# Kernel tuning notes

Hardware: AMD Instinct MI355X
Metric: run time of the kernel (lower is better)

Reference implementation:

```python
import jax, jax.numpy as jnp
import numpy as np

N_NODES = 100000
N_EDGES = 1600000
IN_CH = 128
HID = 128
EMBED = 256
NUM_GRAPHS = 128


def setup_inputs() -> dict:
    key = jax.random.key(0)
    ks = jax.random.split(key, 12)
    x = jax.random.normal(ks[0], (N_NODES, IN_CH), dtype=jnp.float32)
    edge_index = jax.random.randint(ks[1], (2, N_EDGES), 0, N_NODES, dtype=jnp.int64)
    batch = jnp.sort(jax.random.randint(ks[2], (N_NODES,), 0, NUM_GRAPHS, dtype=jnp.int64))
    s = 0.05
    # conv1 MLP: Linear(in_ch,128) -> ReLU -> Linear(128,128)
    W11 = jax.random.normal(ks[3], (IN_CH, HID), dtype=jnp.float32) * s
    b11 = jnp.zeros((HID,), dtype=jnp.float32)
    W12 = jax.random.normal(ks[4], (HID, HID), dtype=jnp.float32) * s
    b12 = jnp.zeros((HID,), dtype=jnp.float32)
    # conv2 MLP: Linear(128,128) -> ReLU -> Linear(128,embed)
    W21 = jax.random.normal(ks[5], (HID, HID), dtype=jnp.float32) * s
    b21 = jnp.zeros((HID,), dtype=jnp.float32)
    W22 = jax.random.normal(ks[6], (HID, EMBED), dtype=jnp.float32) * s
    b22 = jnp.zeros((EMBED,), dtype=jnp.float32)
    gamma = jnp.ones((EMBED,), dtype=jnp.float32)
    beta = jnp.zeros((EMBED,), dtype=jnp.float32)
    return {"x": x, "edge_index": edge_index, "batch": batch,
            "W11": W11, "b11": b11, "W12": W12, "b12": b12,
            "W21": W21, "b21": b21, "W22": W22, "b22": b22,
            "gamma": gamma, "beta": beta}


def _gin_conv(x, src, dst, W_a, b_a, W_b, b_b):
    # GINConv with eps=0: MLP(x + sum_{j in N(i)} x_j)
    msgs = x[src]                                   # [E, d] gather
    agg = jax.ops.segment_sum(msgs, dst, num_segments=N_NODES)  # scatter-add
    h = x + agg
    h = jax.nn.relu(h @ W_a + b_a)
    return h @ W_b + b_b


def reference(x, edge_index, batch, W11, b11, W12, b12, W21, b21, W22, b22, gamma, beta):
    src, dst = edge_index[0], edge_index[1]
    h = jax.nn.relu(_gin_conv(x, src, dst, W11, b11, W12, b12))   # [N, 128]
    h = jax.nn.relu(_gin_conv(h, src, dst, W21, b21, W22, b22))   # [N, 256]
    # global_mean_pool over graphs
    sums = jax.ops.segment_sum(h, batch, num_segments=NUM_GRAPHS)           # [G, 256]
    counts = jax.ops.segment_sum(jnp.ones((N_NODES,), h.dtype), batch, num_segments=NUM_GRAPHS)
    pooled = sums / jnp.maximum(counts, 1.0)[:, None]
    # LayerNorm over last dim (eps=1e-5 as in torch)
    mu = jnp.mean(pooled, axis=-1, keepdims=True)
    var = jnp.var(pooled, axis=-1, keepdims=True)
    out = (pooled - mu) * jax.lax.rsqrt(var + 1e-5) * gamma + beta
    # Dropout in eval mode: identity
    return out
```

## Files before the change

kernel.cpp:

```cpp
#include <hip/hip_runtime.h>

#define GRAPHS 128
#define CHUNKC 4000

typedef _Float16 f16x8 __attribute__((ext_vector_type(8)));
typedef _Float16 f16x4 __attribute__((ext_vector_type(4)));
typedef _Float16 f16x2 __attribute__((ext_vector_type(2)));
typedef float f32x4 __attribute__((ext_vector_type(4)));

__device__ __forceinline__ void fmix_lo(float& a, int w) {
  asm("v_fma_mix_f32 %0, %1, 1.0, %0 op_sel:[0,0,0] op_sel_hi:[1,0,0]" : "+v"(a) : "v"(w));
}
__device__ __forceinline__ void fmix_hi(float& a, int w) {
  asm("v_fma_mix_f32 %0, %1, 1.0, %0 op_sel:[1,0,0] op_sel_hi:[1,0,0]" : "+v"(a) : "v"(w));
}

__device__ __forceinline__ void gload_lds16(const void* g, void* l) {
  __builtin_amdgcn_global_load_lds((const __attribute__((address_space(1))) void*)g,
                                   (__attribute__((address_space(3))) void*)l, 16, 0, 0);
}

__global__ void k_prep(const int* __restrict__ dst, int* __restrict__ histG,
                       int e, int NB, int NW,
                       const float* __restrict__ x, _Float16* __restrict__ P0,
                       _Float16* __restrict__ P1, int n,
                       const float* __restrict__ W11, const float* __restrict__ W12,
                       const float* __restrict__ W21, const float* __restrict__ W22,
                       f16x8* __restrict__ f11, f16x8* __restrict__ f12,
                       f16x8* __restrict__ f21, f16x8* __restrict__ f22,
                       float* __restrict__ pool, int cvtb, int wpb, int poolb) {
  __shared__ int h[256];
  int b = blockIdx.x, t = threadIdx.x;
  if (b < NW) {
    h[t] = 0; __syncthreads();
    int lo = b * CHUNKC, hi = min(lo + CHUNKC, e);
    for (int i = lo + t; i < hi; i += 256) atomicAdd(&h[dst[i] >> 9], 1);
    __syncthreads();
    if (t < NB) histG[t * NW + b] = h[t];
    return;
  }
  b -= NW;
  if (b < cvtb) {
    int i = b * 256 + t;
    if (i < n * 32) {
      float4 v = ((const float4*)x)[i];
      f16x4 hh = { (_Float16)v.x, (_Float16)v.y, (_Float16)v.z, (_Float16)v.w };
      ((f16x4*)P0)[i] = hh;
    }
    return;
  }
  b -= cvtb;
  if (b < wpb) {
    int id = b * 256 + t;
    const float* W; f16x8* F; int C, cid, fshift;
    if (id < 2048)       { W = W11; F = f11; C = 128; cid = id;        fshift = 3; }
    else if (id < 4096)  { W = W12; F = f12; C = 128; cid = id - 2048; fshift = 3; }
    else if (id < 6144)  { W = W21; F = f21; C = 128; cid = id - 4096; fshift = 3; }
    else if (id < 10240) { W = W22; F = f22; C = 256; cid = id - 6144; fshift = 4; }
    else return;
    int lane = cid & 63;
    int rest = cid >> 6;
    int fc = rest & ((1 << fshift) - 1);
    int kk = rest >> fshift;
    int cout = fc * 16 + (lane & 15);
    int kb = kk * 32 + (lane >> 4) * 8;
    f16x8 v;
#pragma unroll
    for (int q = 0; q < 8; ++q) v[q] = (_Float16)W[(size_t)(kb + q) * C + cout];
    F[cid] = v;
    return;
  }
  b -= wpb;
  if (b < poolb) {
    int i = b * 256 + t;
    if (i < GRAPHS * 256) pool[i] = 0.f;
    return;
  }
  if (t < 128) P0[(size_t)n * 128 + t] = (_Float16)0.f;
  else P1[(size_t)n * 128 + (t - 128)] = (_Float16)0.f;
}

__global__ void k_scanA(const int* __restrict__ in, int* __restrict__ out,
                        int* __restrict__ bsum, int N) {
  __shared__ int s[256];
  int t = threadIdx.x, b = blockIdx.x;
  int base = b * 1024 + t * 4;
  int v[4]; int tot = 0;
#pragma unroll
  for (int j = 0; j < 4; ++j) { int i = base + j; v[j] = (i < N) ? in[i] : 0; tot += v[j]; }
  s[t] = tot; __syncthreads();
  for (int o = 1; o < 256; o <<= 1) {
    int x = (t >= o) ? s[t - o] : 0;
    __syncthreads(); s[t] += x; __syncthreads();
  }
  int run = s[t] - tot;
#pragma unroll
  for (int j = 0; j < 4; ++j) { int i = base + j; if (i < N) out[i] = run; run += v[j]; }
  if (t == 255) bsum[b] = s[255];
}

__global__ void k_scanB(int* bsum, int nb, const int* __restrict__ batch,
                        int* __restrict__ starts, int n) {
  __shared__ int s[256];
  int t = threadIdx.x;
  int v = (t < nb) ? bsum[t] : 0;
  s[t] = v; __syncthreads();
  for (int o = 1; o < 256; o <<= 1) {
    int x = (t >= o) ? s[t - o] : 0;
    __syncthreads(); s[t] += x; __syncthreads();
  }
  if (t < nb) bsum[t] = s[t] - v;
  if (t <= GRAPHS) {
    int lo = 0, hi = n;
    while (lo < hi) { int mid = (lo + hi) >> 1; if (batch[mid] < t) lo = mid + 1; else hi = mid; }
    starts[t] = lo;
  }
}

__global__ void k_part(const int* __restrict__ src, const int* __restrict__ dst,
                       const int* __restrict__ histG, const int* __restrict__ off,
                       const int* __restrict__ bsum,
                       int* __restrict__ part, int e, int NB, int NW) {
  __shared__ int hist[256], lbA[256], lbB[256], stmp[256];
  __shared__ int els[CHUNKC];
  int t = threadIdx.x, w = blockIdx.x;
  int hv = (t < NB) ? histG[t * NW + w] : 0;
  hist[t] = hv; stmp[t] = hv; __syncthreads();
  for (int o = 1; o < 256; o <<= 1) {
    int x = (t >= o) ? stmp[t - o] : 0;
    __syncthreads(); stmp[t] += x; __syncthreads();
  }
  lbA[t] = stmp[t] - hv; lbB[t] = stmp[t] - hv;
  __syncthreads();
  int lo = w * CHUNKC, hi = min(lo + CHUNKC, e);
  for (int i = lo + t; i < hi; i += 256) {
    int d = dst[i];
    int p = atomicAdd(&lbB[d >> 9], 1);
    els[p] = src[i] | ((d & 511) << 17);
  }
  __syncthreads();
  int ln = t & 63, wv = t >> 6;
  for (int b = wv; b < NB; b += 4) {
    int c = hist[b], lb = lbA[b];
    int idx = b * NW + w;
    long g = off[idx] + bsum[idx >> 10];
    for (int j = ln; j < c; j += 64) part[g + j] = els[lb + j];
  }
}

__global__ void k_csrb(const int* __restrict__ part, const int* __restrict__ off,
                       const int* __restrict__ bsum,
                       int* __restrict__ ptr, int* __restrict__ csr,
                       int e, int NB, int NW, int n) {
  __shared__ int nh[512], ncur[512], stmp[256];
  int t = threadIdx.x, b = blockIdx.x;
  int i0 = b * NW;
  int s0 = off[i0] + bsum[i0 >> 10];
  int e0 = e;
  if (b + 1 < NB) { int i1 = (b + 1) * NW; e0 = off[i1] + bsum[i1 >> 10]; }
  nh[t] = 0; nh[t + 256] = 0; __syncthreads();
  for (int i = s0 + t; i < e0; i += 256) atomicAdd(&nh[((unsigned)part[i]) >> 17], 1);
  __syncthreads();
  int v0 = nh[2 * t], v1 = nh[2 * t + 1];
  int ps = v0 + v1;
  stmp[t] = ps; __syncthreads();
  for (int o = 1; o < 256; o <<= 1) {
    int x = (t >= o) ? stmp[t - o] : 0;
    __syncthreads(); stmp[t] += x; __syncthreads();
  }
  int base = stmp[t] - ps;
  __syncthreads();
  nh[2 * t] = base;   nh[2 * t + 1] = base + v0;
  ncur[2 * t] = base; ncur[2 * t + 1] = base + v0;
  __syncthreads();
#pragma unroll
  for (int q = 0; q < 2; ++q) {
    int vv = t + q * 256;
    int node = (b << 9) + vv;
    if (node <= n) ptr[node] = s0 + nh[vv];
  }
  for (int i = s0 + t; i < e0; i += 256) {
    int u = part[i];
    int p = atomicAdd(&ncur[((unsigned)u) >> 17], 1);
    csr[s0 + p] = u & 0x1FFFF;
  }
}

__global__ void k_agg_h(const _Float16* __restrict__ in, _Float16* __restrict__ out,
                        const int* __restrict__ ptr, const int* __restrict__ csr, int n) {
  int gid = blockIdx.x * 256 + threadIdx.x;
  int node = gid >> 6, lane = gid & 63;
  if (node >= n) return;
  const f16x8* inp = (const f16x8*)in;
  int cb = lane & 15, rg = lane >> 4;
  f16x8 self = inp[(size_t)node * 16 + cb];
  float acc[8];
#pragma unroll
  for (int c = 0; c < 8; ++c) acc[c] = (rg == 0) ? (float)self[c] : 0.f;
  int s = ptr[node], deg = ptr[node + 1] - s;
  union W { f16x8 v; int i[4]; };
  for (int seg = 0; seg < deg; seg += 64) {
    int my = (seg + lane < deg) ? csr[s + seg + lane] : n;
    int segn = min(deg - seg, 64);
    for (int b2 = 0; b2 < segn; b2 += 32) {
      int jj[8]; W w[8];
#pragma unroll
      for (int u = 0; u < 8; ++u) jj[u] = __shfl(my, b2 + u * 4 + rg);
#pragma unroll
      for (int u = 0; u < 8; ++u) w[u].v = inp[(size_t)jj[u] * 16 + cb];
#pragma unroll
      for (int u = 0; u < 8; ++u)
#pragma unroll
        for (int p = 0; p < 4; ++p) {
          fmix_lo(acc[2 * p], w[u].i[p]);
          fmix_hi(acc[2 * p + 1], w[u].i[p]);
        }
    }
  }
#pragma unroll
  for (int c = 0; c < 8; ++c) {
    acc[c] += __shfl_xor(acc[c], 16);
    acc[c] += __shfl_xor(acc[c], 32);
  }
  if (rg == 0) {
    f16x8 r;
#pragma unroll
    for (int c = 0; c < 8; ++c) r[c] = (_Float16)acc[c];
    ((f16x8*)out)[(size_t)node * 16 + cb] = r;
  }
}

__device__ __forceinline__ f16x8 xpose(f32x4 aE, f32x4 aO, int rg) {
  union U2 { _Float16 h[2]; int i; };
  union U8 { int i[4]; f16x8 v; };
  U2 e01, e23, o01, o23;
  e01.h[0] = (_Float16)aE[0]; e01.h[1] = (_Float16)aE[1];
  e23.h[0] = (_Float16)aE[2]; e23.h[1] = (_Float16)aE[3];
  o01.h[0] = (_Float16)aO[0]; o01.h[1] = (_Float16)aO[1];
  o23.h[0] = (_Float16)aO[2]; o23.h[1] = (_Float16)aO[3];
  int e01x1 = __shfl_xor(e01.i, 16), e01x2 = __shfl_xor(e01.i, 32), e01x3 = __shfl_xor(e01.i, 48);
  int e23x1 = __shfl_xor(e23.i, 16), e23x2 = __shfl_xor(e23.i, 32), e23x3 = __shfl_xor(e23.i, 48);
  int o01x1 = __shfl_xor(o01.i, 16), o01x2 = __shfl_xor(o01.i, 32), o01x3 = __shfl_xor(o01.i, 48);
  int o23x1 = __shfl_xor(o23.i, 16), o23x2 = __shfl_xor(o23.i, 32), o23x3 = __shfl_xor(o23.i, 48);
  U8 r;
  r.i[0] = rg == 0 ? e01.i : rg == 1 ? e01x3 : rg == 2 ? o01x2 : o01x1;
  r.i[1] = rg == 0 ? e23.i : rg == 1 ? e23x3 : rg == 2 ? o23x2 : o23x1;
  r.i[2] = rg == 0 ? e01x1 : rg == 1 ? e01x2 : rg == 2 ? o01x3 : o01.i;
  r.i[3] = rg == 0 ? e23x1 : rg == 1 ? e23x2 : rg == 2 ? o23x3 : o23.i;
  return r.v;
}

__launch_bounds__(256, 2)
__global__ void k_mlp128(const _Float16* __restrict__ in, const f16x8* __restrict__ wfA,
                         const float* __restrict__ bA, const f16x8* __restrict__ wfB,
                         const float* __restrict__ bB, _Float16* __restrict__ out, int n) {
  __shared__ f16x8 wa[2048];
  __shared__ f16x8 wb[2048];
  int t = threadIdx.x;
  int r0 = blockIdx.x * 128;
  int lane = t & 63, w = t >> 6;
  int l16 = lane & 15, rg = lane >> 4;
  int rw = w * 32;
  const f16x8* inp = (const f16x8*)in;
  int ra0 = r0 + rw + l16;      if (ra0 > n) ra0 = n;
  int ra1 = r0 + rw + 16 + l16; if (ra1 > n) ra1 = n;
  f16x8 xf[2][4];
#pragma unroll
  for (int kk = 0; kk < 4; ++kk) {
    xf[0][kk] = inp[(size_t)ra0 * 16 + kk * 4 + rg];
    xf[1][kk] = inp[(size_t)ra1 * 16 + kk * 4 + rg];
  }
#pragma unroll
  for (int i = 0; i < 8; ++i) {
    int base = i * 256 + w * 64;
    gload_lds16(&wfA[base + lane], &wa[base]);
    gload_lds16(&wfB[base + lane], &wb[base]);
  }
  __syncthreads();
  f32x4 acc[2][8];
#pragma unroll
  for (int rs = 0; rs < 2; ++rs)
#pragma unroll
    for (int fc = 0; fc < 8; ++fc) acc[rs][fc] = (f32x4){0.f, 0.f, 0.f, 0.f};
#pragma unroll
  for (int kk = 0; kk < 4; ++kk)
#pragma unroll
    for (int fc = 0; fc < 8; ++fc) {
      f16x8 a = wa[(kk * 8 + fc) * 64 + lane];
      acc[0][fc] = __builtin_amdgcn_mfma_f32_16x16x32_f16(a, xf[0][kk], acc[0][fc], 0, 0, 0);
      acc[1][fc] = __builtin_amdgcn_mfma_f32_16x16x32_f16(a, xf[1][kk], acc[1][fc], 0, 0, 0);
    }
  f16x8 hf[2][4];
#pragma unroll
  for (int fc = 0; fc < 8; ++fc) {
    float4 bv = *(const float4*)(bA + fc * 16 + rg * 4);
#pragma unroll
    for (int rs = 0; rs < 2; ++rs) {
      acc[rs][fc][0] = fmaxf(acc[rs][fc][0] + bv.x, 0.f);
      acc[rs][fc][1] = fmaxf(acc[rs][fc][1] + bv.y, 0.f);
      acc[rs][fc][2] = fmaxf(acc[rs][fc][2] + bv.z, 0.f);
      acc[rs][fc][3] = fmaxf(acc[rs][fc][3] + bv.w, 0.f);
    }
  }
#pragma unroll
  for (int rs = 0; rs < 2; ++rs)
#pragma unroll
    for (int kk = 0; kk < 4; ++kk)
      hf[rs][kk] = xpose(acc[rs][2 * kk], acc[rs][2 * kk + 1], rg);
#pragma unroll
  for (int rs = 0; rs < 2; ++rs)
#pragma unroll
    for (int fc = 0; fc < 8; ++fc) acc[rs][fc] = (f32x4){0.f, 0.f, 0.f, 0.f};
#pragma unroll
  for (int kk = 0; kk < 4; ++kk)
#pragma unroll
    for (int fc = 0; fc < 8; ++fc) {
      f16x8 b = wb[(kk * 8 + fc) * 64 + lane];
      acc[0][fc] = __builtin_amdgcn_mfma_f32_16x16x32_f16(b, hf[0][kk], acc[0][fc], 0, 0, 0);
      acc[1][fc] = __builtin_amdgcn_mfma_f32_16x16x32_f16(b, hf[1][kk], acc[1][fc], 0, 0, 0);
    }
#pragma unroll
  for (int fc = 0; fc < 8; ++fc) {
    float4 bv = *(const float4*)(bB + fc * 16 + rg * 4);
#pragma unroll
    for (int rs = 0; rs < 2; ++rs) {
      acc[rs][fc][0] = fmaxf(acc[rs][fc][0] + bv.x, 0.f);
      acc[rs][fc][1] = fmaxf(acc[rs][fc][1] + bv.y, 0.f);
      acc[rs][fc][2] = fmaxf(acc[rs][fc][2] + bv.z, 0.f);
      acc[rs][fc][3] = fmaxf(acc[rs][fc][3] + bv.w, 0.f);
    }
  }
  f16x8* outp = (f16x8*)out;
#pragma unroll
  for (int rs = 0; rs < 2; ++rs) {
    int row = r0 + rw + rs * 16 + l16;
#pragma unroll
    for (int kk = 0; kk < 4; ++kk) {
      f16x8 o = xpose(acc[rs][2 * kk], acc[rs][2 * kk + 1], rg);
      if (row < n) outp[(size_t)row * 16 + kk * 4 + rg] = o;
    }
  }
}

__launch_bounds__(256, 2)
__global__ void k_mlp_pool(const _Float16* __restrict__ in, const f16x8* __restrict__ wfA,
                           const float* __restrict__ bA, const f16x8* __restrict__ wfB,
                           const float* __restrict__ bB, const int* __restrict__ batch,
                           float* __restrict__ pool, int n) {
  __shared__ f16x8 wa[2048];
  __shared__ f16x8 wb[2048];
  __shared__ float pool_l[8 * 128];
  int t = threadIdx.x;
  int h = blockIdx.x & 1;
  int r0 = (blockIdx.x >> 1) * 128;
  int lane = t & 63, w = t >> 6;
  int l16 = lane & 15, rg = lane >> 4;
  int rw = w * 32;
  const f16x8* inp = (const f16x8*)in;
#pragma unroll
  for (int j = 0; j < 4; ++j) pool_l[j * 256 + t] = 0.f;
  int ra0 = r0 + rw + l16;      if (ra0 > n) ra0 = n;
  int ra1 = r0 + rw + 16 + l16; if (ra1 > n) ra1 = n;
  f16x8 xf[2][4];
#pragma unroll
  for (int kk = 0; kk < 4; ++kk) {
    xf[0][kk] = inp[(size_t)ra0 * 16 + kk * 4 + rg];
    xf[1][kk] = inp[(size_t)ra1 * 16 + kk * 4 + rg];
  }
  int g0 = batch[r0];
  int rloc = rw + rg * 4;
  int g4[2][4];
#pragma unroll
  for (int fr = 0; fr < 2; ++fr)
#pragma unroll
    for (int j = 0; j < 4; ++j) {
      int row = r0 + rloc + fr * 16 + j;
      g4[fr][j] = (row < n) ? batch[row] : -1;
    }
#pragma unroll
  for (int i = 0; i < 8; ++i) {
    int base = i * 256 + w * 64;
    gload_lds16(&wfA[base + lane], &wa[base]);
    int fcl = (i * 4 + w) & 7, kk = (i * 4 + w) >> 3;
    gload_lds16(&wfB[(kk * 16 + h * 8 + fcl) * 64 + lane], &wb[base]);
  }
  __syncthreads();
  f32x4 acc[2][8];
#pragma unroll
  for (int rs = 0; rs < 2; ++rs)
#pragma unroll
    for (int fc = 0; fc < 8; ++fc) acc[rs][fc] = (f32x4){0.f, 0.f, 0.f, 0.f};
#pragma unroll
  for (int kk = 0; kk < 4; ++kk)
#pragma unroll
    for (int fc = 0; fc < 8; ++fc) {
      f16x8 a = wa[(kk * 8 + fc) * 64 + lane];
      acc[0][fc] = __builtin_amdgcn_mfma_f32_16x16x32_f16(a, xf[0][kk], acc[0][fc], 0, 0, 0);
      acc[1][fc] = __builtin_amdgcn_mfma_f32_16x16x32_f16(a, xf[1][kk], acc[1][fc], 0, 0, 0);
    }
  f16x8 hf[2][4];
#pragma unroll
  for (int fc = 0; fc < 8; ++fc) {
    float4 bv = *(const float4*)(bA + fc * 16 + rg * 4);
#pragma unroll
    for (int rs = 0; rs < 2; ++rs) {
      acc[rs][fc][0] = fmaxf(acc[rs][fc][0] + bv.x, 0.f);
      acc[rs][fc][1] = fmaxf(acc[rs][fc][1] + bv.y, 0.f);
      acc[rs][fc][2] = fmaxf(acc[rs][fc][2] + bv.z, 0.f);
      acc[rs][fc][3] = fmaxf(acc[rs][fc][3] + bv.w, 0.f);
    }
  }
#pragma unroll
  for (int rs = 0; rs < 2; ++rs)
#pragma unroll
    for (int kk = 0; kk < 4; ++kk)
      hf[rs][kk] = xpose(acc[rs][2 * kk], acc[rs][2 * kk + 1], rg);
#pragma unroll
  for (int rs = 0; rs < 2; ++rs)
#pragma unroll
    for (int fc = 0; fc < 8; ++fc) acc[rs][fc] = (f32x4){0.f, 0.f, 0.f, 0.f};
#pragma unroll
  for (int kk = 0; kk < 4; ++kk)
#pragma unroll
    for (int fc = 0; fc < 8; ++fc) {
      f16x8 b = wb[(kk * 8 + fc) * 64 + lane];
      acc[0][fc] = __builtin_amdgcn_mfma_f32_16x16x32_f16(hf[0][kk], b, acc[0][fc], 0, 0, 0);
      acc[1][fc] = __builtin_amdgcn_mfma_f32_16x16x32_f16(hf[1][kk], b, acc[1][fc], 0, 0, 0);
    }
#pragma unroll
  for (int fc = 0; fc < 8; ++fc) {
    int col128 = fc * 16 + l16;
    float bv = bB[h * 128 + col128];
#pragma unroll
    for (int fr = 0; fr < 2; ++fr) {
      f32x4 a = acc[fr][fc];
      float run = fmaxf(a[0] + bv, 0.f);
#pragma unroll
      for (int j = 1; j < 4; ++j) {
        float v = fmaxf(a[j] + bv, 0.f);
        if (g4[fr][j] == g4[fr][j - 1]) run += v;
        else {
          int g = g4[fr][j - 1];
          if (g >= 0) {
            int d = g - g0;
            if (d >= 0 && d < 8) atomicAdd(&pool_l[d * 128 + col128], run);
            else atomicAdd(&pool[g * 256 + h * 128 + col128], run);
          }
          run = v;
        }
      }
      int g = g4[fr][3];
      if (g >= 0) {
        int d = g - g0;
        if (d >= 0 && d < 8) atomicAdd(&pool_l[d * 128 + col128], run);
        else atomicAdd(&pool[g * 256 + h * 128 + col128], run);
      }
    }
  }
  __syncthreads();
#pragma unroll
  for (int j = 0; j < 4; ++j) {
    int idx = j * 256 + t;
    int g = g0 + (idx >> 7), col128 = idx & 127;
    float v = pool_l[idx];
    if (g < GRAPHS && v != 0.f) atomicAdd(&pool[g * 256 + h * 128 + col128], v);
  }
}

__global__ void k_final(const float* __restrict__ pool, const int* __restrict__ starts,
                        const float* __restrict__ gamma, const float* __restrict__ beta,
                        float* __restrict__ out) {
  __shared__ float2 red[256];
  int g = blockIdx.x, ch = threadIdx.x;
  int cnt = starts[g + 1] - starts[g];
  float p = pool[g * 256 + ch] / fmaxf((float)cnt, 1.f);
  red[ch] = make_float2(p, p * p);
  __syncthreads();
  for (int off = 128; off > 0; off >>= 1) {
    if (ch < off) { red[ch].x += red[ch + off].x; red[ch].y += red[ch + off].y; }
    __syncthreads();
  }
  float mu = red[0].x * (1.f / 256.f);
  float var = red[0].y * (1.f / 256.f) - mu * mu;
  out[g * 256 + ch] = (p - mu) * rsqrtf(var + 1e-5f) * gamma[ch] + beta[ch];
}

extern "C" void kernel_launch(void* const* d_in, const int* in_sizes, int n_in,
                              void* d_out, int out_size, void* d_ws, size_t ws_size,
                              hipStream_t stream) {
  const float* x     = (const float*)d_in[0];
  const int*   ei    = (const int*)d_in[1];
  const int*   batch = (const int*)d_in[2];
  const float* W11 = (const float*)d_in[3];  const float* b11 = (const float*)d_in[4];
  const float* W12 = (const float*)d_in[5];  const float* b12 = (const float*)d_in[6];
  const float* W21 = (const float*)d_in[7];  const float* b21 = (const float*)d_in[8];
  const float* W22 = (const float*)d_in[9];  const float* b22 = (const float*)d_in[10];
  const float* gamma = (const float*)d_in[11];
  const float* beta  = (const float*)d_in[12];
  float* out = (float*)d_out;

  int n = in_sizes[0] / 128;
  int e = in_sizes[1] / 2;
  const int* src = ei;
  const int* dstv = ei + e;

  int NB = (n + 511) >> 9;
  int NW = (e + CHUNKC - 1) / CHUNKC;
  int NS = NB * NW;
  int mb = (n + 127) / 128;

  char* ws = (char*)d_ws;
  auto alloc = [&](size_t bytes) { char* p = ws; ws += (bytes + 15) & ~(size_t)15; return p; };
  _Float16* P0 = (_Float16*)alloc((size_t)(n + 1) * 128 * 2);
  _Float16* P1 = (_Float16*)alloc((size_t)(n + 1) * 128 * 2);
  float* pool  = (float*)alloc((size_t)GRAPHS * 256 * 4);
  int* ptr     = (int*)alloc((size_t)(n + 1) * 4);
  int* csr     = (int*)alloc((size_t)e * 4);
  int* part    = (int*)alloc((size_t)e * 4);
  int* histG   = (int*)alloc((size_t)NS * 4);
  int* off     = (int*)alloc((size_t)NS * 4);
  int* bsum    = (int*)alloc(256 * 4);
  int* starts  = (int*)alloc((GRAPHS + 1) * 4);
  f16x8* f11 = (f16x8*)alloc(2048 * 16);
  f16x8* f12 = (f16x8*)alloc(2048 * 16);
  f16x8* f21 = (f16x8*)alloc(2048 * 16);
  f16x8* f22 = (f16x8*)alloc(4096 * 16);

  int cvtb = (n * 32 + 255) / 256;
  int wpb = 40;
  int poolb = (GRAPHS * 256 + 255) / 256;
  int prepb = NW + cvtb + wpb + poolb + 1;

  int nbk = (NS + 1023) / 1024;
  k_prep <<<prepb, 256, 0, stream>>>(dstv, histG, e, NB, NW, x, P0, P1, n,
                                     W11, W12, W21, W22, f11, f12, f21, f22,
                                     pool, cvtb, wpb, poolb);
  k_scanA<<<nbk, 256, 0, stream>>>(histG, off, bsum, NS);
  k_scanB<<<1, 256, 0, stream>>>(bsum, nbk, batch, starts, n);
  k_part <<<NW, 256, 0, stream>>>(src, dstv, histG, off, bsum, part, e, NB, NW);
  k_csrb <<<NB, 256, 0, stream>>>(part, off, bsum, ptr, csr, e, NB, NW, n);

  int ab = (n * 64 + 255) / 256;

  k_agg_h<<<ab, 256, 0, stream>>>(P0, P1, ptr, csr, n);
  k_mlp128<<<mb, 256, 0, stream>>>(P1, f11, b11, f12, b12, P0, n);
  k_agg_h<<<ab, 256, 0, stream>>>(P0, P1, ptr, csr, n);
  k_mlp_pool<<<mb * 2, 256, 0, stream>>>(P1, f21, b21, f22, b22, batch, pool, n);
  k_final<<<GRAPHS, 256, 0, stream>>>(pool, starts, gamma, beta, out);
}
```

Before: 282.1 us.

## Fuse neighbor aggregation into MLP kernels and drop separate gather passes

Removes the standalone aggregation kernels and performs the CSR neighbor sum directly inside the MLP kernels, producing MFMA input fragments in registers. The pool kernel now handles both output halves in one block, reloading the second weight half into LDS instead of launching twice as many blocks. This avoids writing and rereading the aggregated feature buffer and two launches, at the cost of far fewer threads doing the gather, each walking neighbor lists serially with limited memory parallelism.

```diff
diff --git a/kernel.cpp b/kernel.cpp
--- a/kernel.cpp
+++ b/kernel.cpp
@@ -5,7 +5,6 @@
 
 typedef _Float16 f16x8 __attribute__((ext_vector_type(8)));
 typedef _Float16 f16x4 __attribute__((ext_vector_type(4)));
-typedef _Float16 f16x2 __attribute__((ext_vector_type(2)));
 typedef float f32x4 __attribute__((ext_vector_type(4)));
 
 __device__ __forceinline__ void fmix_lo(float& a, int w) {
@@ -186,50 +185,6 @@
   }
 }
 
-__global__ void k_agg_h(const _Float16* __restrict__ in, _Float16* __restrict__ out,
-                        const int* __restrict__ ptr, const int* __restrict__ csr, int n) {
-  int gid = blockIdx.x * 256 + threadIdx.x;
-  int node = gid >> 6, lane = gid & 63;
-  if (node >= n) return;
-  const f16x8* inp = (const f16x8*)in;
-  int cb = lane & 15, rg = lane >> 4;
-  f16x8 self = inp[(size_t)node * 16 + cb];
-  float acc[8];
-#pragma unroll
-  for (int c = 0; c < 8; ++c) acc[c] = (rg == 0) ? (float)self[c] : 0.f;
-  int s = ptr[node], deg = ptr[node + 1] - s;
-  union W { f16x8 v; int i[4]; };
-  for (int seg = 0; seg < deg; seg += 64) {
-    int my = (seg + lane < deg) ? csr[s + seg + lane] : n;
-    int segn = min(deg - seg, 64);
-    for (int b2 = 0; b2 < segn; b2 += 32) {
-      int jj[8]; W w[8];
-#pragma unroll
-      for (int u = 0; u < 8; ++u) jj[u] = __shfl(my, b2 + u * 4 + rg);
-#pragma unroll
-      for (int u = 0; u < 8; ++u) w[u].v = inp[(size_t)jj[u] * 16 + cb];
-#pragma unroll
-      for (int u = 0; u < 8; ++u)
-#pragma unroll
-        for (int p = 0; p < 4; ++p) {
-          fmix_lo(acc[2 * p], w[u].i[p]);
-          fmix_hi(acc[2 * p + 1], w[u].i[p]);
-        }
-    }
-  }
-#pragma unroll
-  for (int c = 0; c < 8; ++c) {
-    acc[c] += __shfl_xor(acc[c], 16);
-    acc[c] += __shfl_xor(acc[c], 32);
-  }
-  if (rg == 0) {
-    f16x8 r;
-#pragma unroll
-    for (int c = 0; c < 8; ++c) r[c] = (_Float16)acc[c];
-    ((f16x8*)out)[(size_t)node * 16 + cb] = r;
-  }
-}
-
 __device__ __forceinline__ f16x8 xpose(f32x4 aE, f32x4 aO, int rg) {
   union U2 { _Float16 h[2]; int i; };
   union U8 { int i[4]; f16x8 v; };
@@ -250,10 +205,71 @@
   return r.v;
 }
 
+__device__ __forceinline__ void agg_frag(const f16x8* __restrict__ inp,
+                                         const int* __restrict__ ptr,
+                                         const int* __restrict__ csr,
+                                         int node, int rg, int n, f16x8* xf) {
+  if (node >= n) {
+#pragma unroll
+    for (int kk = 0; kk < 4; ++kk) xf[kk] = (f16x8){0,0,0,0,0,0,0,0};
+    return;
+  }
+  float acc[4][8];
+#pragma unroll
+  for (int kk = 0; kk < 4; ++kk) {
+    f16x8 v = inp[(size_t)node * 16 + kk * 4 + rg];
+#pragma unroll
+    for (int q = 0; q < 8; ++q) acc[kk][q] = (float)v[q];
+  }
+  int s = ptr[node], d = ptr[node + 1] - s;
+  union W { f16x8 v; int i[4]; };
+  int i = 0;
+  for (; i + 2 <= d; i += 2) {
+    int j0 = csr[s + i], j1 = csr[s + i + 1];
+    W a0[4], a1[4];
+#pragma unroll
+    for (int kk = 0; kk < 4; ++kk) {
+      a0[kk].v = inp[(size_t)j0 * 16 + kk * 4 + rg];
+      a1[kk].v = inp[(size_t)j1 * 16 + kk * 4 + rg];
+    }
+#pragma unroll
+    for (int kk = 0; kk < 4; ++kk)
+#pragma unroll
+      for (int p = 0; p < 4; ++p) {
+        fmix_lo(acc[kk][2 * p], a0[kk].i[p]);
+        fmix_hi(acc[kk][2 * p + 1], a0[kk].i[p]);
+        fmix_lo(acc[kk][2 * p], a1[kk].i[p]);
+        fmix_hi(acc[kk][2 * p + 1], a1[kk].i[p]);
+      }
+  }
+  if (i < d) {
+    int j0 = csr[s + i];
+    W a0[4];
+#pragma unroll
+    for (int kk = 0; kk < 4; ++kk) a0[kk].v = inp[(size_t)j0 * 16 + kk * 4 + rg];
+#pragma unroll
+    for (int kk = 0; kk < 4; ++kk)
+#pragma unroll
+      for (int p = 0; p < 4; ++p) {
+        fmix_lo(acc[kk][2 * p], a0[kk].i[p]);
+        fmix_hi(acc[kk][2 * p + 1], a0[kk].i[p]);
+      }
+  }
+#pragma unroll
+  for (int kk = 0; kk < 4; ++kk) {
+    f16x8 r;
+#pragma unroll
+    for (int q = 0; q < 8; ++q) r[q] = (_Float16)acc[kk][q];
+    xf[kk] = r;
+  }
+}
+
 __launch_bounds__(256, 2)
-__global__ void k_mlp128(const _Float16* __restrict__ in, const f16x8* __restrict__ wfA,
-                         const float* __restrict__ bA, const f16x8* __restrict__ wfB,
-                         const float* __restrict__ bB, _Float16* __restrict__ out, int n) {
+__global__ void k_agg_mlp(const _Float16* __restrict__ in, const int* __restrict__ ptr,
+                          const int* __restrict__ csr,
+                          const f16x8* __restrict__ wfA, const float* __restrict__ bA,
+                          const f16x8* __restrict__ wfB, const float* __restrict__ bB,
+                          _Float16* __restrict__ out, int n) {
   __shared__ f16x8 wa[2048];
   __shared__ f16x8 wb[2048];
   int t = threadIdx.x;
@@ -262,20 +278,15 @@
   int l16 = lane & 15, rg = lane >> 4;
   int rw = w * 32;
   const f16x8* inp = (const f16x8*)in;
-  int ra0 = r0 + rw + l16;      if (ra0 > n) ra0 = n;
-  int ra1 = r0 + rw + 16 + l16; if (ra1 > n) ra1 = n;
-  f16x8 xf[2][4];
-#pragma unroll
-  for (int kk = 0; kk < 4; ++kk) {
-    xf[0][kk] = inp[(size_t)ra0 * 16 + kk * 4 + rg];
-    xf[1][kk] = inp[(size_t)ra1 * 16 + kk * 4 + rg];
-  }
 #pragma unroll
   for (int i = 0; i < 8; ++i) {
     int base = i * 256 + w * 64;
     gload_lds16(&wfA[base + lane], &wa[base]);
     gload_lds16(&wfB[base + lane], &wb[base]);
   }
+  f16x8 xf[2][4];
+  agg_frag(inp, ptr, csr, r0 + rw + l16, rg, n, xf[0]);
+  agg_frag(inp, ptr, csr, r0 + rw + 16 + l16, rg, n, xf[1]);
   __syncthreads();
   f32x4 acc[2][8];
 #pragma unroll
@@ -343,29 +354,29 @@
 }
 
 __launch_bounds__(256, 2)
-__global__ void k_mlp_pool(const _Float16* __restrict__ in, const f16x8* __restrict__ wfA,
-                           const float* __restrict__ bA, const f16x8* __restrict__ wfB,
-                           const float* __restrict__ bB, const int* __restrict__ batch,
-                           float* __restrict__ pool, int n) {
+__global__ void k_agg_mlp_pool(const _Float16* __restrict__ in, const int* __restrict__ ptr,
+                               const int* __restrict__ csr,
+                               const f16x8* __restrict__ wfA, const float* __restrict__ bA,
+                               const f16x8* __restrict__ wfB, const float* __restrict__ bB,
+                               const int* __restrict__ batch, float* __restrict__ pool, int n) {
   __shared__ f16x8 wa[2048];
   __shared__ f16x8 wb[2048];
-  __shared__ float pool_l[8 * 128];
+  __shared__ float pool_l[8 * 256];
   int t = threadIdx.x;
-  int h = blockIdx.x & 1;
-  int r0 = (blockIdx.x >> 1) * 128;
+  int r0 = blockIdx.x * 128;
   int lane = t & 63, w = t >> 6;
   int l16 = lane & 15, rg = lane >> 4;
   int rw = w * 32;
   const f16x8* inp = (const f16x8*)in;
 #pragma unroll
-  for (int j = 0; j < 4; ++j) pool_l[j * 256 + t] = 0.f;
-  int ra0 = r0 + rw + l16;      if (ra0 > n) ra0 = n;
-  int ra1 = r0 + rw + 16 + l16; if (ra1 > n) ra1 = n;
-  f16x8 xf[2][4];
-#pragma unroll
-  for (int kk = 0; kk < 4; ++kk) {
-    xf[0][kk] = inp[(size_t)ra0 * 16 + kk * 4 + rg];
-    xf[1][kk] = inp[(size_t)ra1 * 16 + kk * 4 + rg];
+  for (int j = 0; j < 8; ++j) pool_l[j * 256 + t] = 0.f;
+#pragma unroll
+  for (int i = 0; i < 8; ++i) {
+    int base = i * 256 + w * 64;
+    gload_lds16(&wfA[base + lane], &wa[base]);
+    int grp = i * 4 + w;
+    int fcl = grp & 7, kk = grp >> 3;
+    gload_lds16(&wfB[(kk * 16 + fcl) * 64 + lane], &wb[base]);
   }
   int g0 = batch[r0];
   int rloc = rw + rg * 4;
@@ -377,13 +388,9 @@
       int row = r0 + rloc + fr * 16 + j;
       g4[fr][j] = (row < n) ? batch[row] : -1;
     }
-#pragma unroll
-  for (int i = 0; i < 8; ++i) {
-    int base = i * 256 + w * 64;
-    gload_lds16(&wfA[base + lane], &wa[base]);
-    int fcl = (i * 4 + w) & 7, kk = (i * 4 + w) >> 3;
-    gload_lds16(&wfB[(kk * 16 + h * 8 + fcl) * 64 + lane], &wb[base]);
-  }
+  f16x8 xf[2][4];
+  agg_frag(inp, ptr, csr, r0 + rw + l16, rg, n, xf[0]);
+  agg_frag(inp, ptr, csr, r0 + rw + 16 + l16, rg, n, xf[1]);
   __syncthreads();
   f32x4 acc[2][8];
 #pragma unroll
@@ -415,55 +422,68 @@
 #pragma unroll
     for (int kk = 0; kk < 4; ++kk)
       hf[rs][kk] = xpose(acc[rs][2 * kk], acc[rs][2 * kk + 1], rg);
-#pragma unroll
-  for (int rs = 0; rs < 2; ++rs)
-#pragma unroll
-    for (int fc = 0; fc < 8; ++fc) acc[rs][fc] = (f32x4){0.f, 0.f, 0.f, 0.f};
-#pragma unroll
-  for (int kk = 0; kk < 4; ++kk)
+  for (int h = 0; h < 2; ++h) {
+    if (h) {
+      __syncthreads();
+#pragma unroll
+      for (int i = 0; i < 8; ++i) {
+        int base = i * 256 + w * 64;
+        int grp = i * 4 + w;
+        int fcl = grp & 7, kk = grp >> 3;
+        gload_lds16(&wfB[(kk * 16 + 8 + fcl) * 64 + lane], &wb[base]);
+      }
+      __syncthreads();
+    }
+#pragma unroll
+    for (int rs = 0; rs < 2; ++rs)
+#pragma unroll
+      for (int fc = 0; fc < 8; ++fc) acc[rs][fc] = (f32x4){0.f, 0.f, 0.f, 0.f};
+#pragma unroll
+    for (int kk = 0; kk < 4; ++kk)
+#pragma unroll
+      for (int fc = 0; fc < 8; ++fc) {
+        f16x8 b = wb[(kk * 8 + fc) * 64 + lane];
+        acc[0][fc] = __builtin_amdgcn_mfma_f32_16x16x32_f16(hf[0][kk], b, acc[0][fc], 0, 0, 0);
+        acc[1][fc] = __builtin_amdgcn_mfma_f32_16x16x32_f16(hf[1][kk], b, acc[1][fc], 0, 0, 0);
+      }
 #pragma unroll
     for (int fc = 0; fc < 8; ++fc) {
-      f16x8 b = wb[(kk * 8 + fc) * 64 + lane];
-      acc[0][fc] = __builtin_amdgcn_mfma_f32_16x16x32_f16(hf[0][kk], b, acc[0][fc], 0, 0, 0);
-      acc[1][fc] = __builtin_amdgcn_mfma_f32_16x16x32_f16(hf[1][kk], b, acc[1][fc], 0, 0, 0);
-    }
-#pragma unroll
-  for (int fc = 0; fc < 8; ++fc) {
-    int col128 = fc * 16 + l16;
-    float bv = bB[h * 128 + col128];
-#pragma unroll
-    for (int fr = 0; fr < 2; ++fr) {
-      f32x4 a = acc[fr][fc];
-      float run = fmaxf(a[0] + bv, 0.f);
-#pragma unroll
-      for (int j = 1; j < 4; ++j) {
-        float v = fmaxf(a[j] + bv, 0.f);
-        if (g4[fr][j] == g4[fr][j - 1]) run += v;
-        else {
-          int g = g4[fr][j - 1];
-          if (g >= 0) {
-            int d = g - g0;
-            if (d >= 0 && d < 8) atomicAdd(&pool_l[d * 128 + col128], run);
-            else atomicAdd(&pool[g * 256 + h * 128 + col128], run);
+      int col = h * 128 + fc * 16 + l16;
+      float bv = bB[col];
+#pragma unroll
+      for (int fr = 0; fr < 2; ++fr) {
+        f32x4 a = acc[fr][fc];
+        float run = fmaxf(a[0] + bv, 0.f);
+#pragma unroll
+        for (int j = 1; j < 4; ++j) {
+          float v = fmaxf(a[j] + bv, 0.f);
+          if (g4[fr][j] == g4[fr][j - 1]) run += v;
+          else {
+            int g = g4[fr][j - 1];
+            if (g >= 0) {
+              int d = g - g0;
+              if (d >= 0 && d < 8) atomicAdd(&pool_l[d * 256 + col], run);
+              else atomicAdd(&pool[g * 256 + col], run);
+            }
+            run = v;
           }
-          run = v;
+        }
+        int g = g4[fr][3];
+        if (g >= 0) {
+          int d = g - g0;
+          if (d >= 0 && d < 8) atomicAdd(&pool_l[d * 256 + col], run);
+          else atomicAdd(&pool[g * 256 + col], run);
         }
       }
-      int g = g4[fr][3];
-      if (g >= 0) {
-        int d = g - g0;
-        if (d >= 0 && d < 8) atomicAdd(&pool_l[d * 128 + col128], run);
-        else atomicAdd(&pool[g * 256 + h * 128 + col128], run);
-      }
-    }
-  }
-  __syncthreads();
-#pragma unroll
-  for (int j = 0; j < 4; ++j) {
+    }
+  }
+  __syncthreads();
+#pragma unroll
+  for (int j = 0; j < 8; ++j) {
     int idx = j * 256 + t;
-    int g = g0 + (idx >> 7), col128 = idx & 127;
+    int g = g0 + (idx >> 8), col = idx & 255;
     float v = pool_l[idx];
-    if (g < GRAPHS && v != 0.f) atomicAdd(&pool[g * 256 + h * 128 + col128], v);
+    if (g < GRAPHS && v != 0.f) atomicAdd(&pool[g * 256 + col], v);
   }
 }
 
@@ -540,11 +560,7 @@
   k_part <<<NW, 256, 0, stream>>>(src, dstv, histG, off, bsum, part, e, NB, NW);
   k_csrb <<<NB, 256, 0, stream>>>(part, off, bsum, ptr, csr, e, NB, NW, n);
 
-  int ab = (n * 64 + 255) / 256;
-
-  k_agg_h<<<ab, 256, 0, stream>>>(P0, P1, ptr, csr, n);
-  k_mlp128<<<mb, 256, 0, stream>>>(P1, f11, b11, f12, b12, P0, n);
-  k_agg_h<<<ab, 256, 0, stream>>>(P0, P1, ptr, csr, n);
-  k_mlp_pool<<<mb * 2, 256, 0, stream>>>(P1, f21, b21, f22, b22, batch, pool, n);
+  k_agg_mlp<<<mb, 256, 0, stream>>>(P0, ptr, csr, f11, b11, f12, b12, P1, n);
+  k_agg_mlp_pool<<<mb, 256, 0, stream>>>(P1, ptr, csr, f21, b21, f22, b22, batch, pool, n);
   k_final<<<GRAPHS, 256, 0, stream>>>(pool, starts, gamma, beta, out);
 }
```

Measured after the change: 310.6 us. 10.1% more time.

## Process four row tiles per block in MLP kernels to amortize weight loads

Applied to the files above, without the earlier changes.

Each MLP block now loads its weight fragments into LDS once and loops over four consecutive 128-row tiles instead of one, cutting the grid by a factor of four. The direct global-to-LDS loads are replaced by plain register-staged copies. The pool kernel now uses a per-block graph base computed from its first tile for the local pool buffer, and a graph that falls outside that 8-graph window goes to global atomics. The aim is to cut redundant weight traffic and block setup, at the cost of fewer blocks in flight (about 196 for the first MLP) and less latency hiding within each block.

```diff
diff --git a/kernel.cpp b/kernel.cpp
--- a/kernel.cpp
+++ b/kernel.cpp
@@ -5,7 +5,6 @@
 
 typedef _Float16 f16x8 __attribute__((ext_vector_type(8)));
 typedef _Float16 f16x4 __attribute__((ext_vector_type(4)));
-typedef _Float16 f16x2 __attribute__((ext_vector_type(2)));
 typedef float f32x4 __attribute__((ext_vector_type(4)));
 
 __device__ __forceinline__ void fmix_lo(float& a, int w) {
@@ -13,11 +12,6 @@
 }
 __device__ __forceinline__ void fmix_hi(float& a, int w) {
   asm("v_fma_mix_f32 %0, %1, 1.0, %0 op_sel:[1,0,0] op_sel_hi:[1,0,0]" : "+v"(a) : "v"(w));
-}
-
-__device__ __forceinline__ void gload_lds16(const void* g, void* l) {
-  __builtin_amdgcn_global_load_lds((const __attribute__((address_space(1))) void*)g,
-                                   (__attribute__((address_space(3))) void*)l, 16, 0, 0);
 }
 
 __global__ void k_prep(const int* __restrict__ dst, int* __restrict__ histG,
@@ -253,91 +247,97 @@
 __launch_bounds__(256, 2)
 __global__ void k_mlp128(const _Float16* __restrict__ in, const f16x8* __restrict__ wfA,
                          const float* __restrict__ bA, const f16x8* __restrict__ wfB,
-                         const float* __restrict__ bB, _Float16* __restrict__ out, int n) {
+                         const float* __restrict__ bB, _Float16* __restrict__ out,
+                         int n, int mb) {
   __shared__ f16x8 wa[2048];
   __shared__ f16x8 wb[2048];
   int t = threadIdx.x;
-  int r0 = blockIdx.x * 128;
   int lane = t & 63, w = t >> 6;
   int l16 = lane & 15, rg = lane >> 4;
   int rw = w * 32;
   const f16x8* inp = (const f16x8*)in;
-  int ra0 = r0 + rw + l16;      if (ra0 > n) ra0 = n;
-  int ra1 = r0 + rw + 16 + l16; if (ra1 > n) ra1 = n;
-  f16x8 xf[2][4];
-#pragma unroll
-  for (int kk = 0; kk < 4; ++kk) {
-    xf[0][kk] = inp[(size_t)ra0 * 16 + kk * 4 + rg];
-    xf[1][kk] = inp[(size_t)ra1 * 16 + kk * 4 + rg];
-  }
+  f16x8* outp = (f16x8*)out;
 #pragma unroll
   for (int i = 0; i < 8; ++i) {
-    int base = i * 256 + w * 64;
-    gload_lds16(&wfA[base + lane], &wa[base]);
-    gload_lds16(&wfB[base + lane], &wb[base]);
-  }
-  __syncthreads();
-  f32x4 acc[2][8];
-#pragma unroll
-  for (int rs = 0; rs < 2; ++rs)
-#pragma unroll
-    for (int fc = 0; fc < 8; ++fc) acc[rs][fc] = (f32x4){0.f, 0.f, 0.f, 0.f};
-#pragma unroll
-  for (int kk = 0; kk < 4; ++kk)
+    wa[t + i * 256] = wfA[t + i * 256];
+    wb[t + i * 256] = wfB[t + i * 256];
+  }
+  __syncthreads();
+  int t0 = blockIdx.x * 4;
+#pragma unroll 1
+  for (int it = 0; it < 4; ++it) {
+    int tile = t0 + it;
+    if (tile >= mb) break;
+    int r0 = tile * 128;
+    int ra0 = r0 + rw + l16;      if (ra0 > n) ra0 = n;
+    int ra1 = r0 + rw + 16 + l16; if (ra1 > n) ra1 = n;
+    f16x8 xf[2][4];
+#pragma unroll
+    for (int kk = 0; kk < 4; ++kk) {
+      xf[0][kk] = inp[(size_t)ra0 * 16 + kk * 4 + rg];
+      xf[1][kk] = inp[(size_t)ra1 * 16 + kk * 4 + rg];
+    }
+    f32x4 acc[2][8];
+#pragma unroll
+    for (int rs = 0; rs < 2; ++rs)
+#pragma unroll
+      for (int fc = 0; fc < 8; ++fc) acc[rs][fc] = (f32x4){0.f, 0.f, 0.f, 0.f};
+#pragma unroll
+    for (int kk = 0; kk < 4; ++kk)
+#pragma unroll
+      for (int fc = 0; fc < 8; ++fc) {
+        f16x8 a = wa[(kk * 8 + fc) * 64 + lane];
+        acc[0][fc] = __builtin_amdgcn_mfma_f32_16x16x32_f16(a, xf[0][kk], acc[0][fc], 0, 0, 0);
+        acc[1][fc] = __builtin_amdgcn_mfma_f32_16x16x32_f16(a, xf[1][kk], acc[1][fc], 0, 0, 0);
+      }
+    f16x8 hf[2][4];
 #pragma unroll
     for (int fc = 0; fc < 8; ++fc) {
-      f16x8 a = wa[(kk * 8 + fc) * 64 + lane];
-      acc[0][fc] = __builtin_amdgcn_mfma_f32_16x16x32_f16(a, xf[0][kk], acc[0][fc], 0, 0, 0);
-      acc[1][fc] = __builtin_amdgcn_mfma_f32_16x16x32_f16(a, xf[1][kk], acc[1][fc], 0, 0, 0);
-    }
-  f16x8 hf[2][4];
-#pragma unroll
-  for (int fc = 0; fc < 8; ++fc) {
-    float4 bv = *(const float4*)(bA + fc * 16 + rg * 4);
+      float4 bv = *(const float4*)(bA + fc * 16 + rg * 4);
+#pragma unroll
+      for (int rs = 0; rs < 2; ++rs) {
+        acc[rs][fc][0] = fmaxf(acc[rs][fc][0] + bv.x, 0.f);
+        acc[rs][fc][1] = fmaxf(acc[rs][fc][1] + bv.y, 0.f);
+        acc[rs][fc][2] = fmaxf(acc[rs][fc][2] + bv.z, 0.f);
+        acc[rs][fc][3] = fmaxf(acc[rs][fc][3] + bv.w, 0.f);
+      }
+    }
+#pragma unroll
+    for (int rs = 0; rs < 2; ++rs)
+#pragma unroll
+      for (int kk = 0; kk < 4; ++kk)
+        hf[rs][kk] = xpose(acc[rs][2 * kk], acc[rs][2 * kk + 1], rg);
+#pragma unroll
+    for (int rs = 0; rs < 2; ++rs)
+#pragma unroll
+      for (int fc = 0; fc < 8; ++fc) acc[rs][fc] = (f32x4){0.f, 0.f, 0.f, 0.f};
+#pragma unroll
+    for (int kk = 0; kk < 4; ++kk)
+#pragma unroll
+      for (int fc = 0; fc < 8; ++fc) {
+        f16x8 b = wb[(kk * 8 + fc) * 64 + lane];
+        acc[0][fc] = __builtin_amdgcn_mfma_f32_16x16x32_f16(b, hf[0][kk], acc[0][fc], 0, 0, 0);
+        acc[1][fc] = __builtin_amdgcn_mfma_f32_16x16x32_f16(b, hf[1][kk], acc[1][fc], 0, 0, 0);
+      }
+#pragma unroll
+    for (int fc = 0; fc < 8; ++fc) {
+      float4 bv = *(const float4*)(bB + fc * 16 + rg * 4);
+#pragma unroll
+      for (int rs = 0; rs < 2; ++rs) {
+        acc[rs][fc][0] = fmaxf(acc[rs][fc][0] + bv.x, 0.f);
+        acc[rs][fc][1] = fmaxf(acc[rs][fc][1] + bv.y, 0.f);
+        acc[rs][fc][2] = fmaxf(acc[rs][fc][2] + bv.z, 0.f);
+        acc[rs][fc][3] = fmaxf(acc[rs][fc][3] + bv.w, 0.f);
+      }
+    }
 #pragma unroll
     for (int rs = 0; rs < 2; ++rs) {
-      acc[rs][fc][0] = fmaxf(acc[rs][fc][0] + bv.x, 0.f);
-      acc[rs][fc][1] = fmaxf(acc[rs][fc][1] + bv.y, 0.f);
-      acc[rs][fc][2] = fmaxf(acc[rs][fc][2] + bv.z, 0.f);
-      acc[rs][fc][3] = fmaxf(acc[rs][fc][3] + bv.w, 0.f);
-    }
-  }
-#pragma unroll
-  for (int rs = 0; rs < 2; ++rs)
-#pragma unroll
-    for (int kk = 0; kk < 4; ++kk)
-      hf[rs][kk] = xpose(acc[rs][2 * kk], acc[rs][2 * kk + 1], rg);
-#pragma unroll
-  for (int rs = 0; rs < 2; ++rs)
-#pragma unroll
-    for (int fc = 0; fc < 8; ++fc) acc[rs][fc] = (f32x4){0.f, 0.f, 0.f, 0.f};
-#pragma unroll
-  for (int kk = 0; kk < 4; ++kk)
-#pragma unroll
-    for (int fc = 0; fc < 8; ++fc) {
-      f16x8 b = wb[(kk * 8 + fc) * 64 + lane];
-      acc[0][fc] = __builtin_amdgcn_mfma_f32_16x16x32_f16(b, hf[0][kk], acc[0][fc], 0, 0, 0);
-      acc[1][fc] = __builtin_amdgcn_mfma_f32_16x16x32_f16(b, hf[1][kk], acc[1][fc], 0, 0, 0);
-    }
-#pragma unroll
-  for (int fc = 0; fc < 8; ++fc) {
-    float4 bv = *(const float4*)(bB + fc * 16 + rg * 4);
-#pragma unroll
-    for (int rs = 0; rs < 2; ++rs) {
-      acc[rs][fc][0] = fmaxf(acc[rs][fc][0] + bv.x, 0.f);
-      acc[rs][fc][1] = fmaxf(acc[rs][fc][1] + bv.y, 0.f);
-      acc[rs][fc][2] = fmaxf(acc[rs][fc][2] + bv.z, 0.f);
-      acc[rs][fc][3] = fmaxf(acc[rs][fc][3] + bv.w, 0.f);
-    }
-  }
-  f16x8* outp = (f16x8*)out;
-#pragma unroll
-  for (int rs = 0; rs < 2; ++rs) {
-    int row = r0 + rw + rs * 16 + l16;
-#pragma unroll
-    for (int kk = 0; kk < 4; ++kk) {
-      f16x8 o = xpose(acc[rs][2 * kk], acc[rs][2 * kk + 1], rg);
-      if (row < n) outp[(size_t)row * 16 + kk * 4 + rg] = o;
+      int row = r0 + rw + rs * 16 + l16;
+#pragma unroll
+      for (int kk = 0; kk < 4; ++kk) {
+        f16x8 o = xpose(acc[rs][2 * kk], acc[rs][2 * kk + 1], rg);
+        if (row < n) outp[(size_t)row * 16 + kk * 4 + rg] = o;
+      }
     }
   }
 }
@@ -346,114 +346,122 @@
 __global__ void k_mlp_pool(const _Float16* __restrict__ in, const f16x8* __restrict__ wfA,
                            const float* __restrict__ bA, const f16x8* __restrict__ wfB,
                            const float* __restrict__ bB, const int* __restrict__ batch,
-                           float* __restrict__ pool, int n) {
+                           float* __restrict__ pool, int n, int mb) {
   __shared__ f16x8 wa[2048];
   __shared__ f16x8 wb[2048];
   __shared__ float pool_l[8 * 128];
   int t = threadIdx.x;
   int h = blockIdx.x & 1;
-  int r0 = (blockIdx.x >> 1) * 128;
+  int slot = blockIdx.x >> 1;
   int lane = t & 63, w = t >> 6;
   int l16 = lane & 15, rg = lane >> 4;
   int rw = w * 32;
   const f16x8* inp = (const f16x8*)in;
 #pragma unroll
   for (int j = 0; j < 4; ++j) pool_l[j * 256 + t] = 0.f;
-  int ra0 = r0 + rw + l16;      if (ra0 > n) ra0 = n;
-  int ra1 = r0 + rw + 16 + l16; if (ra1 > n) ra1 = n;
-  f16x8 xf[2][4];
-#pragma unroll
-  for (int kk = 0; kk < 4; ++kk) {
-    xf[0][kk] = inp[(size_t)ra0 * 16 + kk * 4 + rg];
-    xf[1][kk] = inp[(size_t)ra1 * 16 + kk * 4 + rg];
-  }
-  int g0 = batch[r0];
-  int rloc = rw + rg * 4;
-  int g4[2][4];
-#pragma unroll
-  for (int fr = 0; fr < 2; ++fr)
-#pragma unroll
-    for (int j = 0; j < 4; ++j) {
-      int row = r0 + rloc + fr * 16 + j;
-      g4[fr][j] = (row < n) ? batch[row] : -1;
-    }
 #pragma unroll
   for (int i = 0; i < 8; ++i) {
-    int base = i * 256 + w * 64;
-    gload_lds16(&wfA[base + lane], &wa[base]);
-    int fcl = (i * 4 + w) & 7, kk = (i * 4 + w) >> 3;
-    gload_lds16(&wfB[(kk * 16 + h * 8 + fcl) * 64 + lane], &wb[base]);
-  }
-  __syncthreads();
-  f32x4 acc[2][8];
-#pragma unroll
-  for (int rs = 0; rs < 2; ++rs)
-#pragma unroll
-    for (int fc = 0; fc < 8; ++fc) acc[rs][fc] = (f32x4){0.f, 0.f, 0.f, 0.f};
-#pragma unroll
-  for (int kk = 0; kk < 4; ++kk)
+    int id = t + i * 256;
+    int lj = id & 63, fcl = (id >> 6) & 7, kk = id >> 9;
+    wa[id] = wfA[id];
+    wb[id] = wfB[(kk * 16 + h * 8 + fcl) * 64 + lj];
+  }
+  int t0 = slot * 4;
+  int r0B = t0 * 128; if (r0B >= n) r0B = n - 1;
+  int g0B = batch[r0B];
+  __syncthreads();
+#pragma unroll 1
+  for (int it = 0; it < 4; ++it) {
+    int tile = t0 + it;
+    if (tile >= mb) break;
+    int r0 = tile * 128;
+    int ra0 = r0 + rw + l16;      if (ra0 > n) ra0 = n;
+    int ra1 = r0 + rw + 16 + l16; if (ra1 > n) ra1 = n;
+    f16x8 xf[2][4];
+#pragma unroll
+    for (int kk = 0; kk < 4; ++kk) {
+      xf[0][kk] = inp[(size_t)ra0 * 16 + kk * 4 + rg];
+      xf[1][kk] = inp[(size_t)ra1 * 16 + kk * 4 + rg];
+    }
+    int rloc = rw + rg * 4;
+    int g4[2][4];
+#pragma unroll
+    for (int fr = 0; fr < 2; ++fr)
+#pragma unroll
+      for (int j = 0; j < 4; ++j) {
+        int row = r0 + rloc + fr * 16 + j;
+        g4[fr][j] = (row < n) ? batch[row] : -1;
+      }
+    f32x4 acc[2][8];
+#pragma unroll
+    for (int rs = 0; rs < 2; ++rs)
+#pragma unroll
+      for (int fc = 0; fc < 8; ++fc) acc[rs][fc] = (f32x4){0.f, 0.f, 0.f, 0.f};
+#pragma unroll
+    for (int kk = 0; kk < 4; ++kk)
+#pragma unroll
+      for (int fc = 0; fc < 8; ++fc) {
+        f16x8 a = wa[(kk * 8 + fc) * 64 + lane];
+        acc[0][fc] = __builtin_amdgcn_mfma_f32_16x16x32_f16(a, xf[0][kk], acc[0][fc], 0, 0, 0);
+        acc[1][fc] = __builtin_amdgcn_mfma_f32_16x16x32_f16(a, xf[1][kk], acc[1][fc], 0, 0, 0);
+      }
+    f16x8 hf[2][4];
 #pragma unroll
     for (int fc = 0; fc < 8; ++fc) {
-      f16x8 a = wa[(kk * 8 + fc) * 64 + lane];
-      acc[0][fc] = __builtin_amdgcn_mfma_f32_16x16x32_f16(a, xf[0][kk], acc[0][fc], 0, 0, 0);
-      acc[1][fc] = __builtin_amdgcn_mfma_f32_16x16x32_f16(a, xf[1][kk], acc[1][fc], 0, 0, 0);
-    }
-  f16x8 hf[2][4];
-#pragma unroll
-  for (int fc = 0; fc < 8; ++fc) {
-    float4 bv = *(const float4*)(bA + fc * 16 + rg * 4);
-#pragma unroll
-    for (int rs = 0; rs < 2; ++rs) {
-      acc[rs][fc][0] = fmaxf(acc[rs][fc][0] + bv.x, 0.f);
-      acc[rs][fc][1] = fmaxf(acc[rs][fc][1] + bv.y, 0.f);
-      acc[rs][fc][2] = fmaxf(acc[rs][fc][2] + bv.z, 0.f);
-      acc[rs][fc][3] = fmaxf(acc[rs][fc][3] + bv.w, 0.f);
-    }
-  }
-#pragma unroll
-  for (int rs = 0; rs < 2; ++rs)
+      float4 bv = *(const float4*)(bA + fc * 16 + rg * 4);
+#pragma unroll
+      for (int rs = 0; rs < 2; ++rs) {
+        acc[rs][fc][0] = fmaxf(acc[rs][fc][0] + bv.x, 0.f);
+        acc[rs][fc][1] = fmaxf(acc[rs][fc][1] + bv.y, 0.f);
+        acc[rs][fc][2] = fmaxf(acc[rs][fc][2] + bv.z, 0.f);
+        acc[rs][fc][3] = fmaxf(acc[rs][fc][3] + bv.w, 0.f);
+      }
+    }
+#pragma unroll
+    for (int rs = 0; rs < 2; ++rs)
+#pragma unroll
+      for (int kk = 0; kk < 4; ++kk)
+        hf[rs][kk] = xpose(acc[rs][2 * kk], acc[rs][2 * kk + 1], rg);
+#pragma unroll
+    for (int rs = 0; rs < 2; ++rs)
+#pragma unroll
+      for (int fc = 0; fc < 8; ++fc) acc[rs][fc] = (f32x4){0.f, 0.f, 0.f, 0.f};
 #pragma unroll
     for (int kk = 0; kk < 4; ++kk)
-      hf[rs][kk] = xpose(acc[rs][2 * kk], acc[rs][2 * kk + 1], rg);
-#pragma unroll
-  for (int rs = 0; rs < 2; ++rs)
-#pragma unroll
-    for (int fc = 0; fc < 8; ++fc) acc[rs][fc] = (f32x4){0.f, 0.f, 0.f, 0.f};
-#pragma unroll
-  for (int kk = 0; kk < 4; ++kk)
+#pragma unroll
+      for (int fc = 0; fc < 8; ++fc) {
+        f16x8 b = wb[(kk * 8 + fc) * 64 + lane];
+        acc[0][fc] = __builtin_amdgcn_mfma_f32_16x16x32_f16(hf[0][kk], b, acc[0][fc], 0, 0, 0);
+        acc[1][fc] = __builtin_amdgcn_mfma_f32_16x16x32_f16(hf[1][kk], b, acc[1][fc], 0, 0, 0);
+      }
 #pragma unroll
     for (int fc = 0; fc < 8; ++fc) {
-      f16x8 b = wb[(kk * 8 + fc) * 64 + lane];
-      acc[0][fc] = __builtin_amdgcn_mfma_f32_16x16x32_f16(hf[0][kk], b, acc[0][fc], 0, 0, 0);
-      acc[1][fc] = __builtin_amdgcn_mfma_f32_16x16x32_f16(hf[1][kk], b, acc[1][fc], 0, 0, 0);
-    }
-#pragma unroll
-  for (int fc = 0; fc < 8; ++fc) {
-    int col128 = fc * 16 + l16;
-    float bv = bB[h * 128 + col128];
-#pragma unroll
-    for (int fr = 0; fr < 2; ++fr) {
-      f32x4 a = acc[fr][fc];
-      float run = fmaxf(a[0] + bv, 0.f);
-#pragma unroll
-      for (int j = 1; j < 4; ++j) {
-        float v = fmaxf(a[j] + bv, 0.f);
-        if (g4[fr][j] == g4[fr][j - 1]) run += v;
-        else {
-          int g = g4[fr][j - 1];
-          if (g >= 0) {
-            int d = g - g0;
-            if (d >= 0 && d < 8) atomicAdd(&pool_l[d * 128 + col128], run);
-            else atomicAdd(&pool[g * 256 + h * 128 + col128], run);
+      int col128 = fc * 16 + l16;
+      float bv = bB[h * 128 + col128];
+#pragma unroll
+      for (int fr = 0; fr < 2; ++fr) {
+        f32x4 a = acc[fr][fc];
+        float run = fmaxf(a[0] + bv, 0.f);
+#pragma unroll
+        for (int j = 1; j < 4; ++j) {
+          float v = fmaxf(a[j] + bv, 0.f);
+          if (g4[fr][j] == g4[fr][j - 1]) run += v;
+          else {
+            int g = g4[fr][j - 1];
+            if (g >= 0) {
+              int d = g - g0B;
+              if (d >= 0 && d < 8) atomicAdd(&pool_l[d * 128 + col128], run);
+              else atomicAdd(&pool[g * 256 + h * 128 + col128], run);
+            }
+            run = v;
           }
-          run = v;
         }
-      }
-      int g = g4[fr][3];
-      if (g >= 0) {
-        int d = g - g0;
-        if (d >= 0 && d < 8) atomicAdd(&pool_l[d * 128 + col128], run);
-        else atomicAdd(&pool[g * 256 + h * 128 + col128], run);
+        int g = g4[fr][3];
+        if (g >= 0) {
+          int d = g - g0B;
+          if (d >= 0 && d < 8) atomicAdd(&pool_l[d * 128 + col128], run);
+          else atomicAdd(&pool[g * 256 + h * 128 + col128], run);
+        }
       }
     }
   }
@@ -461,7 +469,7 @@
 #pragma unroll
   for (int j = 0; j < 4; ++j) {
     int idx = j * 256 + t;
-    int g = g0 + (idx >> 7), col128 = idx & 127;
+    int g = g0B + (idx >> 7), col128 = idx & 127;
     float v = pool_l[idx];
     if (g < GRAPHS && v != 0.f) atomicAdd(&pool[g * 256 + h * 128 + col128], v);
   }
@@ -508,6 +516,7 @@
   int NW = (e + CHUNKC - 1) / CHUNKC;
   int NS = NB * NW;
   int mb = (n + 127) / 128;
+  int slots = (mb + 3) / 4;
 
   char* ws = (char*)d_ws;
   auto alloc = [&](size_t bytes) { char* p = ws; ws += (bytes + 15) & ~(size_t)15; return p; };
@@ -543,8 +552,8 @@
   int ab = (n * 64 + 255) / 256;
 
   k_agg_h<<<ab, 256, 0, stream>>>(P0, P1, ptr, csr, n);
-  k_mlp128<<<mb, 256, 0, stream>>>(P1, f11, b11, f12, b12, P0, n);
+  k_mlp128<<<slots, 256, 0, stream>>>(P1, f11, b11, f12, b12, P0, n, mb);
   k_agg_h<<<ab, 256, 0, stream>>>(P0, P1, ptr, csr, n);
-  k_mlp_pool<<<mb * 2, 256, 0, stream>>>(P1, f21, b21, f22, b22, batch, pool, n);
+  k_mlp_pool<<<slots * 2, 256, 0, stream>>>(P1, f21, b21, f22, b22, batch, pool, n, mb);
   k_final<<<GRAPHS, 256, 0, stream>>>(pool, starts, gamma, beta, out);
 }
```

Measured after the change: 285.0 us. Within noise of the previous version (+1.0%).
